# Kernel optimization log

Hardware: AMD Instinct MI355X
Metric: run time of the kernel (lower is better)

The kernel has to match this reference:

```python
import jax, jax.numpy as jnp
import numpy as np

N, E, NC, ES, NT, G = 200000, 500000, 150000, 350000, 100000, 1024
FN, FE, H, T = 133, 14, 128, 3


def _enc_params(key, prefix):
    ks = jax.random.split(key, 4)
    g = lambda k, shape, fan_in: jax.random.normal(k, shape, jnp.float32) / np.sqrt(fan_in).astype(np.float32)
    return {
        f"{prefix}_w_node": g(ks[0], (FN, H), FN),
        f"{prefix}_b_node": jnp.zeros((H,), jnp.float32),
        f"{prefix}_w_edge": g(ks[1], (FE, H), FE),
        f"{prefix}_b_edge": jnp.zeros((H,), jnp.float32),
        f"{prefix}_w_mp": g(ks[2], (T, H, H), H),
        f"{prefix}_b_mp": jnp.zeros((T, H), jnp.float32),
        f"{prefix}_w_out": g(ks[3], (H, H), H),
        f"{prefix}_b_out": jnp.zeros((H,), jnp.float32),
    }


def setup_inputs() -> dict:
    key = jax.random.key(0)
    k = lambda i: jax.random.fold_in(key, i)
    inp = {
        "x": jax.random.normal(k(0), (N, FN), jnp.float32),
        "node_weight": jax.random.uniform(k(1), (N,), jnp.float32),
        "edge_index": jax.random.randint(k(2), (2, E), 0, N),
        "edge_attr": jax.random.normal(k(3), (E, FE), jnp.float32),
        "edge_weight": jax.random.uniform(k(4), (E,), jnp.float32),
        "batch": jnp.sort(jax.random.randint(k(5), (N,), 0, G)),
        "context_nodes_mapper": jax.random.randint(k(6), (NC,), 0, N),
        "target_nodes_mapper": jax.random.randint(k(7), (NT,), 0, N),
        "combined_subgraphs": jax.random.randint(k(8), (2, ES), 0, NC),
        "subgraphs_edges_mapper": jax.random.randint(k(9), (ES,), 0, E),
        "context_edges_mask": jax.random.bernoulli(k(10), 0.7, (ES,)),
    }
    inp.update(_enc_params(k(11), "ctx"))
    inp.update(_enc_params(k(12), "tgt"))
    return inp


def wd_mpnn(x, src, dst, edge_attr, edge_weight, node_weight,
            w_node, b_node, w_edge, b_edge, w_mp, b_mp, w_out, b_out, n_nodes):
    # Weighted-edge node MPNN: gather source node states, combine with edge
    # embedding, scale by edge weight, scatter-sum onto destination nodes.
    h = jax.nn.relu(x @ w_node + b_node)                 # [n_nodes, H]
    eh = jax.nn.relu(edge_attr @ w_edge + b_edge)        # [n_edges, H]
    ew = edge_weight[:, None]
    for t in range(w_mp.shape[0]):
        msg = ew * (h[src] + eh)                         # gather [n_edges, H]
        agg = jax.ops.segment_sum(msg, dst, num_segments=n_nodes)
        h = jax.nn.relu(h + agg @ w_mp[t] + b_mp[t])
    return (h @ w_out + b_out) * node_weight[:, None]


def segment_mean(vals, seg, num_segments):
    s = jax.ops.segment_sum(vals, seg, num_segments=num_segments)
    c = jax.ops.segment_sum(jnp.ones((vals.shape[0],), vals.dtype), seg, num_segments=num_segments)
    return s / jnp.maximum(c, 1.0)[:, None]


def reference(x, node_weight, edge_index, edge_attr, edge_weight, batch,
              context_nodes_mapper, target_nodes_mapper, combined_subgraphs,
              subgraphs_edges_mapper, context_edges_mask,
              ctx_w_node, ctx_b_node, ctx_w_edge, ctx_b_edge, ctx_w_mp, ctx_b_mp, ctx_w_out, ctx_b_out,
              tgt_w_node, tgt_b_node, tgt_w_edge, tgt_b_edge, tgt_w_mp, tgt_b_mp, tgt_w_out, tgt_b_out):
    # --- context branch: gather subgraph node/edge features ---
    cx = x[context_nodes_mapper]                         # [NC, FN]
    cnw = node_weight[context_nodes_mapper]              # [NC]
    cea = edge_attr[subgraphs_edges_mapper]              # [ES, FE]
    # boolean edge mask folded into edge weights (messages scale linearly in
    # edge_weight, so zeroing masked edges == dropping them) -> jit friendly
    cew = edge_weight[subgraphs_edges_mapper] * context_edges_mask.astype(jnp.float32)
    csrc, cdst = combined_subgraphs[0], combined_subgraphs[1]
    ctx_nodes = wd_mpnn(cx, csrc, cdst, cea, cew, cnw,
                        ctx_w_node, ctx_b_node, ctx_w_edge, ctx_b_edge,
                        ctx_w_mp, ctx_b_mp, ctx_w_out, ctx_b_out, NC)
    ctx_emb = segment_mean(ctx_nodes, batch[context_nodes_mapper], G)   # [G, H]

    # --- target branch: full-graph encode, pool over target nodes ---
    full = wd_mpnn(x, edge_index[0], edge_index[1], edge_attr, edge_weight, node_weight,
                   tgt_w_node, tgt_b_node, tgt_w_edge, tgt_b_edge,
                   tgt_w_mp, tgt_b_mp, tgt_w_out, tgt_b_out, N)
    tgt_emb = segment_mean(full[target_nodes_mapper], batch[target_nodes_mapper], G)  # [G, H]

    return jnp.stack([ctx_emb, tgt_emb])                 # [2, G, H]
```

## Files before the change

kernel.cpp:

```cpp
#include <hip/hip_runtime.h>
#include <hip/hip_fp16.h>
#include <stdint.h>

#define H 128
#define FN 133
#define FE 14
#define NG 1024
#define APAD 133

typedef float v2f __attribute__((ext_vector_type(2)));

__device__ __forceinline__ uint2 pack_half4(float4 v) {
    __half2 a = __float22half2_rn(make_float2(v.x, v.y));
    __half2 b = __float22half2_rn(make_float2(v.z, v.w));
    uint2 r;
    r.x = *reinterpret_cast<unsigned int*>(&a);
    r.y = *reinterpret_cast<unsigned int*>(&b);
    return r;
}
__device__ __forceinline__ float4 unpack_half4(uint2 u) {
    __half2 a = *reinterpret_cast<__half2*>(&u.x);
    __half2 b = *reinterpret_cast<__half2*>(&u.y);
    float2 fa = __half22float2(a);
    float2 fb = __half22float2(b);
    return make_float4(fa.x, fa.y, fb.x, fb.y);
}

__global__ void k_sniff(const unsigned int* __restrict__ w, int nwords, int* __restrict__ flag) {
    __shared__ int sawFloat, sawBig;
    if (threadIdx.x == 0) { sawFloat = 0; sawBig = 0; }
    __syncthreads();
    int f = 0, bg = 0;
    for (int i = threadIdx.x; i < nwords; i += blockDim.x) {
        unsigned int v = w[i];
        if (v == 0u || v == 1u) continue;
        if (v == 0x3F800000u) f = 1; else bg = 1;
    }
    if (f) atomicOr(&sawFloat, 1);
    if (bg) atomicOr(&sawBig, 1);
    __syncthreads();
    if (threadIdx.x == 0) *flag = sawBig ? 1 : (sawFloat ? 2 : 0);
}

__device__ __forceinline__ float mask_val(const void* mask, int mm, long e) {
    if (mm == 1)      return ((const unsigned char*)mask)[e] ? 1.f : 0.f;
    else if (mm == 2) return ((const float*)mask)[e];
    else              return ((const int*)mask)[e] ? 1.f : 0.f;
}

template<bool GATHER>
__global__ __launch_bounds__(256)
void k_gemm_enc(const float* __restrict__ x, const int* __restrict__ map, int nrows,
                const float* __restrict__ w, const float* __restrict__ bias,
                float* __restrict__ hout) {
    __shared__ float w_lds[32][H];
    __shared__ float a_lds[32][APAD];
    __shared__ int   m_lds[128];
    const int tid = threadIdx.x;
    const int rbase = blockIdx.x * 128;
    if (GATHER && tid < 128) {
        int row = rbase + tid;
        m_lds[tid] = (row < nrows) ? map[row] : 0;
    }
    const int tx = tid & 15, ty = tid >> 4;
    float acc[8][8] = {};
    for (int kc = 0; kc < 5; ++kc) {
        const int k0 = kc * 32;
        __syncthreads();
        for (int i = tid; i < 32 * 32; i += 256) {
            int kk = i >> 5, c4 = i & 31;
            float4 v = make_float4(0.f, 0.f, 0.f, 0.f);
            if (k0 + kk < FN)
                v = reinterpret_cast<const float4*>(w + (size_t)(k0 + kk) * H)[c4];
            *reinterpret_cast<float4*>(&w_lds[kk][c4 * 4]) = v;
        }
        for (int i = tid; i < 128 * 32; i += 256) {
            int r = i >> 5, kk = i & 31;
            int row = rbase + r;
            float v = 0.f;
            if (row < nrows && k0 + kk < FN) {
                int sr = GATHER ? m_lds[r] : row;
                v = x[(size_t)sr * FN + k0 + kk];
            }
            a_lds[kk][r] = v;
        }
        __syncthreads();
        #pragma unroll 4
        for (int k = 0; k < 32; ++k) {
            float4 a0 = *reinterpret_cast<const float4*>(&a_lds[k][ty * 8]);
            float4 a1 = *reinterpret_cast<const float4*>(&a_lds[k][ty * 8 + 4]);
            float4 w0 = *reinterpret_cast<const float4*>(&w_lds[k][tx * 4]);
            float4 w1 = *reinterpret_cast<const float4*>(&w_lds[k][64 + tx * 4]);
            float aa[8] = {a0.x, a0.y, a0.z, a0.w, a1.x, a1.y, a1.z, a1.w};
            float ww[8] = {w0.x, w0.y, w0.z, w0.w, w1.x, w1.y, w1.z, w1.w};
            #pragma unroll
            for (int i2 = 0; i2 < 8; ++i2)
                #pragma unroll
                for (int j = 0; j < 8; ++j)
                    acc[i2][j] += aa[i2] * ww[j];
        }
    }
    float4 b0 = *reinterpret_cast<const float4*>(bias + tx * 4);
    float4 b1 = *reinterpret_cast<const float4*>(bias + 64 + tx * 4);
    float bb[8] = {b0.x, b0.y, b0.z, b0.w, b1.x, b1.y, b1.z, b1.w};
    #pragma unroll
    for (int i2 = 0; i2 < 8; ++i2) {
        int row = rbase + ty * 8 + i2;
        if (row < nrows) {
            float4 o0, o1;
            o0.x = fmaxf(acc[i2][0] + bb[0], 0.f); o0.y = fmaxf(acc[i2][1] + bb[1], 0.f);
            o0.z = fmaxf(acc[i2][2] + bb[2], 0.f); o0.w = fmaxf(acc[i2][3] + bb[3], 0.f);
            o1.x = fmaxf(acc[i2][4] + bb[4], 0.f); o1.y = fmaxf(acc[i2][5] + bb[5], 0.f);
            o1.z = fmaxf(acc[i2][6] + bb[6], 0.f); o1.w = fmaxf(acc[i2][7] + bb[7], 0.f);
            float* hp = hout + (size_t)row * H + tx * 4;
            *reinterpret_cast<float4*>(hp)      = o0;
            *reinterpret_cast<float4*>(hp + 64) = o1;
        }
    }
}

template<int MODE>
__global__ __launch_bounds__(256)
void k_hist(const int* __restrict__ dst, const float* __restrict__ edge_weight,
            const int* __restrict__ emap, const void* __restrict__ mask,
            const int* __restrict__ mmode_p, int* __restrict__ deg, int nedges) {
    int e = blockIdx.x * 256 + threadIdx.x;
    if (e >= nedges) return;
    int eo = MODE ? emap[e] : e;
    float w = edge_weight[eo];
    if (MODE) w *= mask_val(mask, *mmode_p, e);
    if (w != 0.f) atomicAdd(&deg[dst[e]], 1);
}

__global__ __launch_bounds__(256)
void k_scan1(const int* __restrict__ deg, int* __restrict__ off, int* __restrict__ bsum, int n) {
    __shared__ int tsum[256];
    const int tid = threadIdx.x;
    const int base = blockIdx.x * 1024;
    int local[4]; int s = 0;
    #pragma unroll
    for (int j = 0; j < 4; ++j) {
        int i = base + tid * 4 + j;
        local[j] = (i < n) ? deg[i] : 0;
        s += local[j];
    }
    tsum[tid] = s;
    __syncthreads();
    for (int d = 1; d < 256; d <<= 1) {
        int v = (tid >= d) ? tsum[tid - d] : 0;
        __syncthreads();
        tsum[tid] += v;
        __syncthreads();
    }
    int excl = tsum[tid] - s;
    #pragma unroll
    for (int j = 0; j < 4; ++j) {
        int i = base + tid * 4 + j;
        if (i < n) off[i] = excl;
        excl += local[j];
    }
    if (tid == 255) bsum[blockIdx.x] = tsum[255];
}

__global__ __launch_bounds__(256)
void k_scan2(int* __restrict__ bsum, int nb) {
    __shared__ int tsum[256];
    const int tid = threadIdx.x;
    int local[4]; int s = 0;
    #pragma unroll
    for (int j = 0; j < 4; ++j) {
        int i = tid * 4 + j;
        local[j] = (i < nb) ? bsum[i] : 0;
        s += local[j];
    }
    tsum[tid] = s;
    __syncthreads();
    for (int d = 1; d < 256; d <<= 1) {
        int v = (tid >= d) ? tsum[tid - d] : 0;
        __syncthreads();
        tsum[tid] += v;
        __syncthreads();
    }
    int excl = tsum[tid] - s;
    #pragma unroll
    for (int j = 0; j < 4; ++j) {
        int i = tid * 4 + j;
        if (i < nb) bsum[i] = excl;
        excl += local[j];
    }
}

__global__ __launch_bounds__(256)
void k_scan3(const int* __restrict__ bsum, int* __restrict__ off, int* __restrict__ cur, int n) {
    int i = blockIdx.x * 256 + threadIdx.x;
    if (i < n) {
        int o = off[i] + bsum[i >> 10];
        off[i] = o;
        cur[i] = o;
    }
}

template<int MODE>
__global__ __launch_bounds__(256)
void k_scatter(const int* __restrict__ src, const int* __restrict__ dst,
               const float* __restrict__ edge_weight,
               const int* __restrict__ emap, const void* __restrict__ mask,
               const int* __restrict__ mmode_p, int* __restrict__ cur,
               int2* __restrict__ epk, int2* __restrict__ epkh,
               int nedges) {
    int e = blockIdx.x * 256 + threadIdx.x;
    if (e >= nedges) return;
    int eo = MODE ? emap[e] : e;
    float w = edge_weight[eo];
    if (MODE) w *= mask_val(mask, *mmode_p, e);
    if (w != 0.f) {
        int pos = atomicAdd(&cur[dst[e]], 1);
        int wb = __float_as_int(w);
        epk[pos]  = make_int2(src[e], wb);
        epkh[pos] = make_int2(eo, wb);
    }
}

__global__ __launch_bounds__(256)
void k_mark(const int* __restrict__ rowmap, int* __restrict__ nflag, int nrows) {
    int r = blockIdx.x * 256 + threadIdx.x;
    if (r < nrows) nflag[rowmap[r]] = 1;
}

__global__ __launch_bounds__(256)
void k_compact(const int* __restrict__ nflag, int* __restrict__ list,
               int* __restrict__ cnt, int n) {
    int i = blockIdx.x * 256 + threadIdx.x;
    bool p = (i < n) && (nflag[i] != 0);
    unsigned long long m = __ballot(p);
    int lane = threadIdx.x & 63;
    int wcount = __popcll(m);
    int base = 0;
    if (lane == 0 && wcount) base = atomicAdd(cnt, wcount);
    base = __shfl(base, 0, 64);
    if (p) {
        int pos = base + (int)__popcll(m & ((1ull << lane) - 1ull));
        list[pos] = i;
    }
}

__global__ __launch_bounds__(256)
void k_msg_eh(const int* __restrict__ off, const int* __restrict__ deg,
              const int2* __restrict__ epk, const int2* __restrict__ epkh,
              const float* __restrict__ edge_attr,
              const float* __restrict__ w_edge, const float* __restrict__ b_edge,
              const float* __restrict__ h,
              __half* __restrict__ agg, __half* __restrict__ aggeh, int nnodes) {
    __shared__ float we_lds[FE * H];
    __shared__ float be_lds[H];
    for (int i = threadIdx.x; i < FE * H; i += 256) we_lds[i] = w_edge[i];
    if (threadIdx.x < H) be_lds[threadIdx.x] = b_edge[threadIdx.x];
    __syncthreads();
    const int hw = threadIdx.x >> 5;
    const int ln = threadIdx.x & 31;
    const int c  = ln * 4;
    int v = blockIdx.x * 8 + hw;
    if (v >= nnodes) return;
    v2f acc0 = {0.f, 0.f}, acc1 = {0.f, 0.f};
    v2f aeh0 = {0.f, 0.f}, aeh1 = {0.f, 0.f};
    const int o = off[v], d = deg[v];
    const float4 bev = *reinterpret_cast<const float4*>(be_lds + c);
    const v2f bev0 = {bev.x, bev.y}, bev1 = {bev.z, bev.w};
    for (int jb = 0; jb < d; jb += 32) {
        const int nn = min(32, d - jb);
        int2 m1 = make_int2(0, 0), m2 = make_int2(0, 0);
        if (ln < nn) { m1 = epk[o + jb + ln]; m2 = epkh[o + jb + ln]; }
        const int msrc = m1.x;
        const int meo  = m2.x;
        const float mw = __int_as_float(m1.y);
        for (int q = 0; q < nn; q += 2) {
            int   s0 = __shfl(msrc, q, 32);
            int   e0 = __shfl(meo,  q, 32);
            float w0 = __shfl(mw,   q, 32);
            int   s1 = __shfl(msrc, q + 1, 32);
            int   e1 = __shfl(meo,  q + 1, 32);
            float w1 = __shfl(mw,   q + 1, 32);
            if (q + 1 >= nn) { s1 = s0; e1 = e0; w1 = 0.f; }
            float4 hv0 = *reinterpret_cast<const float4*>(h + (size_t)s0 * H + c);
            float4 hv1 = *reinterpret_cast<const float4*>(h + (size_t)s1 * H + c);
            float a0 = (ln < FE) ? edge_attr[(size_t)e0 * FE + ln] : 0.f;
            float a1 = (ln < FE) ? edge_attr[(size_t)e1 * FE + ln] : 0.f;
            v2f eh00 = bev0, eh01 = bev1, eh10 = bev0, eh11 = bev1;
            #pragma unroll
            for (int k = 0; k < FE; ++k) {
                float f0 = __shfl(a0, k, 32);
                float f1 = __shfl(a1, k, 32);
                float4 wv = *reinterpret_cast<const float4*>(we_lds + k * H + c);
                v2f wva = {wv.x, wv.y}, wvb = {wv.z, wv.w};
                v2f f0v = {f0, f0}, f1v = {f1, f1};
                eh00 += f0v * wva; eh01 += f0v * wvb;
                eh10 += f1v * wva; eh11 += f1v * wvb;
            }
            v2f r00 = {w0 * fmaxf(eh00.x, 0.f), w0 * fmaxf(eh00.y, 0.f)};
            v2f r01 = {w0 * fmaxf(eh01.x, 0.f), w0 * fmaxf(eh01.y, 0.f)};
            v2f r10 = {w1 * fmaxf(eh10.x, 0.f), w1 * fmaxf(eh10.y, 0.f)};
            v2f r11 = {w1 * fmaxf(eh11.x, 0.f), w1 * fmaxf(eh11.y, 0.f)};
            aeh0 += r00 + r10; aeh1 += r01 + r11;
            v2f w0v = {w0, w0}, w1v = {w1, w1};
            acc0 += w0v * (v2f){hv0.x, hv0.y} + w1v * (v2f){hv1.x, hv1.y} + r00 + r10;
            acc1 += w0v * (v2f){hv0.z, hv0.w} + w1v * (v2f){hv1.z, hv1.w} + r01 + r11;
        }
    }
    *reinterpret_cast<uint2*>(agg   + (size_t)v * H + c) = pack_half4(make_float4(acc0.x, acc0.y, acc1.x, acc1.y));
    *reinterpret_cast<uint2*>(aggeh + (size_t)v * H + c) = pack_half4(make_float4(aeh0.x, aeh0.y, aeh1.x, aeh1.y));
}

template<int LIST>
__global__ __launch_bounds__(256)
void k_msg_csr(const int* __restrict__ off, const int* __restrict__ deg,
               const int2* __restrict__ epk, const __half* __restrict__ aggeh,
               const float* __restrict__ h, __half* __restrict__ agg,
               const int* __restrict__ list, const int* __restrict__ cnt_p,
               int nnodes) {
    const int hw = threadIdx.x >> 5;
    const int ln = threadIdx.x & 31;
    const int c  = ln * 4;
    int i = blockIdx.x * 8 + hw;
    int bound = LIST ? *cnt_p : nnodes;
    if (i >= bound) return;
    int v = LIST ? list[i] : i;
    float4 a0 = unpack_half4(*reinterpret_cast<const uint2*>(aggeh + (size_t)v * H + c));
    v2f acc0 = {a0.x, a0.y}, acc1 = {a0.z, a0.w};
    const int o = off[v], d = deg[v];
    for (int jb = 0; jb < d; jb += 32) {
        const int nn = min(32, d - jb);
        int2 meta = make_int2(0, 0);
        if (ln < nn) meta = epk[o + jb + ln];
        const int ms = meta.x;
        const float mw = __int_as_float(meta.y);
        for (int q = 0; q < nn; q += 4) {
            #pragma unroll
            for (int u = 0; u < 4; ++u) {
                int qq = q + u;
                int   s = __shfl(ms, qq, 32);
                float w = __shfl(mw, qq, 32);
                if (qq >= nn) { s = 0; w = 0.f; }
                float4 hv = *reinterpret_cast<const float4*>(h + (size_t)s * H + c);
                v2f wv = {w, w};
                acc0 += wv * (v2f){hv.x, hv.y};
                acc1 += wv * (v2f){hv.z, hv.w};
            }
        }
    }
    *reinterpret_cast<uint2*>(agg + (size_t)v * H + c) = pack_half4(make_float4(acc0.x, acc0.y, acc1.x, acc1.y));
}

template<int LIST>
__global__ __launch_bounds__(256)
void k_gemm_update(const __half* __restrict__ agg, int nrows,
                   const float* __restrict__ w, const float* __restrict__ bias,
                   float* __restrict__ h,
                   const int* __restrict__ list, const int* __restrict__ cnt_p) {
    __shared__ float w_lds[32][H];
    __shared__ float a_lds[32][APAD];
    __shared__ int   m_lds[128];
    const int tid = threadIdx.x;
    const int rbase = blockIdx.x * 128;
    const int bound = LIST ? *cnt_p : nrows;
    if (rbase >= bound) return;
    if (LIST && tid < 128) {
        int r = rbase + tid;
        m_lds[tid] = (r < bound) ? list[r] : 0;
    }
    const int tx = tid & 15, ty = tid >> 4;
    float acc[8][8] = {};
    for (int kc = 0; kc < 4; ++kc) {
        const int k0 = kc * 32;
        __syncthreads();
        for (int i = tid; i < 1024; i += 256) {
            int kk = i >> 5, c4 = i & 31;
            *reinterpret_cast<float4*>(&w_lds[kk][c4 * 4]) =
                reinterpret_cast<const float4*>(w + (size_t)(k0 + kk) * H)[c4];
        }
        for (int i = tid; i < 1024; i += 256) {
            int r = i >> 3, f = i & 7;
            int row = rbase + r;
            float4 v = make_float4(0.f, 0.f, 0.f, 0.f);
            if (row < bound) {
                int hr = LIST ? m_lds[r] : row;
                v = unpack_half4(reinterpret_cast<const uint2*>(agg + (size_t)hr * H + k0)[f]);
            }
            a_lds[f * 4 + 0][r] = v.x;
            a_lds[f * 4 + 1][r] = v.y;
            a_lds[f * 4 + 2][r] = v.z;
            a_lds[f * 4 + 3][r] = v.w;
        }
        __syncthreads();
        #pragma unroll 4
        for (int k = 0; k < 32; ++k) {
            float4 a0 = *reinterpret_cast<const float4*>(&a_lds[k][ty * 8]);
            float4 a1 = *reinterpret_cast<const float4*>(&a_lds[k][ty * 8 + 4]);
            float4 w0 = *reinterpret_cast<const float4*>(&w_lds[k][tx * 4]);
            float4 w1 = *reinterpret_cast<const float4*>(&w_lds[k][64 + tx * 4]);
            float aa[8] = {a0.x, a0.y, a0.z, a0.w, a1.x, a1.y, a1.z, a1.w};
            float ww[8] = {w0.x, w0.y, w0.z, w0.w, w1.x, w1.y, w1.z, w1.w};
            #pragma unroll
            for (int i2 = 0; i2 < 8; ++i2)
                #pragma unroll
                for (int j = 0; j < 8; ++j)
                    acc[i2][j] += aa[i2] * ww[j];
        }
    }
    float4 b0 = *reinterpret_cast<const float4*>(bias + tx * 4);
    float4 b1 = *reinterpret_cast<const float4*>(bias + 64 + tx * 4);
    float bb[8] = {b0.x, b0.y, b0.z, b0.w, b1.x, b1.y, b1.z, b1.w};
    #pragma unroll
    for (int i2 = 0; i2 < 8; ++i2) {
        int row = rbase + ty * 8 + i2;
        if (row < bound) {
            int hr = LIST ? m_lds[ty * 8 + i2] : row;
            float* hp = h + (size_t)hr * H + tx * 4;
            float4 h0 = *reinterpret_cast<const float4*>(hp);
            float4 h1 = *reinterpret_cast<const float4*>(hp + 64);
            float4 o0, o1;
            o0.x = fmaxf(h0.x + acc[i2][0] + bb[0], 0.f); o0.y = fmaxf(h0.y + acc[i2][1] + bb[1], 0.f);
            o0.z = fmaxf(h0.z + acc[i2][2] + bb[2], 0.f); o0.w = fmaxf(h0.w + acc[i2][3] + bb[3], 0.f);
            o1.x = fmaxf(h1.x + acc[i2][4] + bb[4], 0.f); o1.y = fmaxf(h1.y + acc[i2][5] + bb[5], 0.f);
            o1.z = fmaxf(h1.z + acc[i2][6] + bb[6], 0.f); o1.w = fmaxf(h1.w + acc[i2][7] + bb[7], 0.f);
            *reinterpret_cast<float4*>(hp)      = o0;
            *reinterpret_cast<float4*>(hp + 64) = o1;
        }
    }
}

__global__ __launch_bounds__(256)
void k_ghist(const int* __restrict__ rowmap, const int* __restrict__ batch,
             int* __restrict__ deg_g, int nrows) {
    int r = blockIdx.x * 256 + threadIdx.x;
    if (r < nrows) atomicAdd(&deg_g[batch[rowmap[r]]], 1);
}

__global__ __launch_bounds__(256)
void k_gscan(const int* __restrict__ deg, int* __restrict__ off, int* __restrict__ cur) {
    __shared__ int tsum[256];
    const int tid = threadIdx.x;
    int local[4]; int s = 0;
    #pragma unroll
    for (int j = 0; j < 4; ++j) { local[j] = deg[tid * 4 + j]; s += local[j]; }
    tsum[tid] = s;
    __syncthreads();
    for (int d = 1; d < 256; d <<= 1) {
        int v = (tid >= d) ? tsum[tid - d] : 0;
        __syncthreads();
        tsum[tid] += v;
        __syncthreads();
    }
    int excl = tsum[tid] - s;
    #pragma unroll
    for (int j = 0; j < 4; ++j) {
        off[tid * 4 + j] = excl;
        cur[tid * 4 + j] = excl;
        excl += local[j];
    }
}

template<bool GATHER>
__global__ __launch_bounds__(256)
void k_gscatter(const int* __restrict__ rowmap, const int* __restrict__ batch,
                const float* __restrict__ nodew, int* __restrict__ cur,
                int* __restrict__ prow, float* __restrict__ pnw, int nrows) {
    int r = blockIdx.x * 256 + threadIdx.x;
    if (r >= nrows) return;
    int oid = rowmap[r];
    int g = batch[oid];
    int pos = atomicAdd(&cur[g], 1);
    prow[pos] = GATHER ? oid : r;
    pnw[pos]  = nodew[oid];
}

__global__ __launch_bounds__(256)
void k_pool(const int* __restrict__ off_g, const int* __restrict__ deg_g,
            const int* __restrict__ prow, const float* __restrict__ pnw,
            const float* __restrict__ h,
            const float* __restrict__ w, const float* __restrict__ bias,
            float* __restrict__ outp) {
    __shared__ float s_lds[4][H];
    __shared__ float ssum[H];
    __shared__ float r_lds[2][H];
    __shared__ float cg_lds[4];
    const int g = blockIdx.x;
    const int o = off_g[g], cnt = deg_g[g];
    const int wv = threadIdx.x >> 6, lane = threadIdx.x & 63;
    float ax = 0.f, ay = 0.f, cg = 0.f;
    for (int i = wv; i < cnt; i += 4) {
        int hrow = prow[o + i];
        float nw = pnw[o + i];
        float2 v = *reinterpret_cast<const float2*>(h + (size_t)hrow * H + lane * 2);
        ax += nw * v.x; ay += nw * v.y; cg += nw;
    }
    s_lds[wv][lane * 2]     = ax;
    s_lds[wv][lane * 2 + 1] = ay;
    if (lane == 0) cg_lds[wv] = cg;
    __syncthreads();
    if (threadIdx.x < H)
        ssum[threadIdx.x] = s_lds[0][threadIdx.x] + s_lds[1][threadIdx.x]
                          + s_lds[2][threadIdx.x] + s_lds[3][threadIdx.x];
    __syncthreads();
    const int c = threadIdx.x & 127, kh = threadIdx.x >> 7;
    float p = 0.f;
    #pragma unroll 8
    for (int k = 0; k < 64; ++k)
        p += ssum[kh * 64 + k] * w[(size_t)(kh * 64 + k) * H + c];
    r_lds[kh][c] = p;
    __syncthreads();
    if (threadIdx.x < H) {
        float cga = cg_lds[0] + cg_lds[1] + cg_lds[2] + cg_lds[3];
        float val = r_lds[0][c] + r_lds[1][c] + bias[c] * cga;
        outp[(size_t)g * H + c] = val / fmaxf((float)cnt, 1.f);
    }
}

extern "C" void kernel_launch(void* const* d_in, const int* in_sizes, int n_in,
                              void* d_out, int out_size, void* d_ws, size_t ws_size,
                              hipStream_t stream) {
    (void)n_in; (void)out_size; (void)ws_size;
    const float* x           = (const float*)d_in[0];
    const float* node_weight = (const float*)d_in[1];
    const int*   edge_index  = (const int*)d_in[2];
    const float* edge_attr   = (const float*)d_in[3];
    const float* edge_weight = (const float*)d_in[4];
    const int*   batch       = (const int*)d_in[5];
    const int*   cnm         = (const int*)d_in[6];
    const int*   tnm         = (const int*)d_in[7];
    const int*   csub        = (const int*)d_in[8];
    const int*   sem         = (const int*)d_in[9];
    const void*  cmask       = d_in[10];

    const float* ctx_w_node = (const float*)d_in[11];
    const float* ctx_b_node = (const float*)d_in[12];
    const float* ctx_w_edge = (const float*)d_in[13];
    const float* ctx_b_edge = (const float*)d_in[14];
    const float* ctx_w_mp   = (const float*)d_in[15];
    const float* ctx_b_mp   = (const float*)d_in[16];
    const float* ctx_w_out  = (const float*)d_in[17];
    const float* ctx_b_out  = (const float*)d_in[18];
    const float* tgt_w_node = (const float*)d_in[19];
    const float* tgt_b_node = (const float*)d_in[20];
    const float* tgt_w_edge = (const float*)d_in[21];
    const float* tgt_b_edge = (const float*)d_in[22];
    const float* tgt_w_mp   = (const float*)d_in[23];
    const float* tgt_b_mp   = (const float*)d_in[24];
    const float* tgt_w_out  = (const float*)d_in[25];
    const float* tgt_b_out  = (const float*)d_in[26];

    const int N  = in_sizes[1];
    const int E  = in_sizes[4];
    const int NC = in_sizes[6];
    const int NT = in_sizes[7];
    const int ES = in_sizes[9];
    const int NMAX = (NT > NC) ? NT : NC;

    float* out = (float*)d_out;

    char* ws = (char*)d_ws;
    float*  h     = (float*)ws;  ws += (size_t)N * H * sizeof(float);
    __half* agg   = (__half*)ws; ws += (size_t)N * H * sizeof(__half);
    __half* aggeh = (__half*)ws; ws += (size_t)N * H * sizeof(__half);
    int2*  epk    = (int2*)ws;   ws += (size_t)E * sizeof(int2);
    int2*  epkh   = (int2*)ws;   ws += (size_t)E * sizeof(int2);
    int*   deg    = (int*)ws;    ws += (size_t)N * sizeof(int);
    int*   off    = (int*)ws;    ws += (size_t)N * sizeof(int);
    int*   cur    = (int*)ws;    ws += (size_t)N * sizeof(int);
    int*   nflag  = (int*)ws;    ws += (size_t)N * sizeof(int);
    int*   ncnt   = (int*)ws;    ws += sizeof(int);
    int*   nlist  = (int*)ws;    ws += (size_t)N * sizeof(int);
    int*   bsum   = (int*)ws;    ws += 1024 * sizeof(int);
    int*   deg_g  = (int*)ws;    ws += NG * sizeof(int);
    int*   off_g  = (int*)ws;    ws += NG * sizeof(int);
    int*   cur_g  = (int*)ws;    ws += NG * sizeof(int);
    int*   prow   = (int*)ws;    ws += (size_t)NMAX * sizeof(int);
    float* pnw    = (float*)ws;  ws += (size_t)NMAX * sizeof(float);
    int*   flag   = (int*)ws;    ws += sizeof(int);

    int nwords = ES / 4; if (nwords > 8192) nwords = 8192;
    k_sniff<<<1, 256, 0, stream>>>((const unsigned int*)cmask, nwords, flag);

    {
        const int* fsrc = edge_index;
        const int* fdst = edge_index + E;
        hipMemsetAsync(deg, 0, (size_t)N * sizeof(int), stream);
        hipMemsetAsync(nflag, 0, ((size_t)N + 1) * sizeof(int), stream);
        int egrid = (E + 255) / 256;
        k_hist<0><<<egrid, 256, 0, stream>>>(fdst, edge_weight, nullptr, nullptr, nullptr, deg, E);
        int nb1 = (N + 1023) / 1024;
        k_scan1<<<nb1, 256, 0, stream>>>(deg, off, bsum, N);
        k_scan2<<<1, 256, 0, stream>>>(bsum, nb1);
        k_scan3<<<(N + 255) / 256, 256, 0, stream>>>(bsum, off, cur, N);
        k_scatter<0><<<egrid, 256, 0, stream>>>(fsrc, fdst, edge_weight, nullptr, nullptr, nullptr,
                                                cur, epk, epkh, E);
        k_mark<<<(NT + 255) / 256, 256, 0, stream>>>(tnm, nflag, NT);
        k_compact<<<(N + 255) / 256, 256, 0, stream>>>(nflag, nlist, ncnt, N);

        k_gemm_enc<false><<<(N + 127) / 128, 256, 0, stream>>>(x, nullptr, N, tgt_w_node, tgt_b_node, h);
        k_msg_eh<<<(N + 7) / 8, 256, 0, stream>>>(off, deg, epk, epkh, edge_attr,
                                                  tgt_w_edge, tgt_b_edge, h, agg, aggeh, N);
        k_gemm_update<0><<<(N + 127) / 128, 256, 0, stream>>>(agg, N, tgt_w_mp, tgt_b_mp, h,
                                                              nullptr, nullptr);
        k_msg_csr<0><<<(N + 7) / 8, 256, 0, stream>>>(off, deg, epk, aggeh, h, agg, nullptr, nullptr, N);
        k_gemm_update<0><<<(N + 127) / 128, 256, 0, stream>>>(agg, N, tgt_w_mp + H * H, tgt_b_mp + H, h,
                                                              nullptr, nullptr);
        k_msg_csr<1><<<(N + 7) / 8, 256, 0, stream>>>(off, deg, epk, aggeh, h, agg, nlist, ncnt, N);
        k_gemm_update<1><<<(N + 127) / 128, 256, 0, stream>>>(agg, N, tgt_w_mp + 2 * H * H, tgt_b_mp + 2 * H, h,
                                                              nlist, ncnt);
        hipMemsetAsync(deg_g, 0, NG * sizeof(int), stream);
        k_ghist<<<(NT + 255) / 256, 256, 0, stream>>>(tnm, batch, deg_g, NT);
        k_gscan<<<1, 256, 0, stream>>>(deg_g, off_g, cur_g);
        k_gscatter<true><<<(NT + 255) / 256, 256, 0, stream>>>(tnm, batch, node_weight, cur_g, prow, pnw, NT);
        k_pool<<<NG, 256, 0, stream>>>(off_g, deg_g, prow, pnw, h, tgt_w_out, tgt_b_out,
                                       out + (size_t)NG * H);
    }

    {
        const int* csrc = csub;
        const int* cdst = csub + ES;
        hipMemsetAsync(deg, 0, (size_t)NC * sizeof(int), stream);
        int egrid = (ES + 255) / 256;
        k_hist<1><<<egrid, 256, 0, stream>>>(cdst, edge_weight, sem, cmask, flag, deg, ES);
        int nb1 = (NC + 1023) / 1024;
        k_scan1<<<nb1, 256, 0, stream>>>(deg, off, bsum, NC);
        k_scan2<<<1, 256, 0, stream>>>(bsum, nb1);
        k_scan3<<<(NC + 255) / 256, 256, 0, stream>>>(bsum, off, cur, NC);
        k_scatter<1><<<egrid, 256, 0, stream>>>(csrc, cdst, edge_weight, sem, cmask, flag,
                                                cur, epk, epkh, ES);
        k_gemm_enc<true><<<(NC + 127) / 128, 256, 0, stream>>>(x, cnm, NC, ctx_w_node, ctx_b_node, h);
        k_msg_eh<<<(NC + 7) / 8, 256, 0, stream>>>(off, deg, epk, epkh, edge_attr,
                                                   ctx_w_edge, ctx_b_edge, h, agg, aggeh, NC);
        k_gemm_update<0><<<(NC + 127) / 128, 256, 0, stream>>>(agg, NC, ctx_w_mp, ctx_b_mp, h,
                                                               nullptr, nullptr);
        for (int t = 1; t < 3; ++t) {
            k_msg_csr<0><<<(NC + 7) / 8, 256, 0, stream>>>(off, deg, epk, aggeh, h, agg, nullptr, nullptr, NC);
            k_gemm_update<0><<<(NC + 127) / 128, 256, 0, stream>>>(agg, NC,
                                                                   ctx_w_mp + t * H * H, ctx_b_mp + t * H, h,
                                                                   nullptr, nullptr);
        }
        hipMemsetAsync(deg_g, 0, NG * sizeof(int), stream);
        k_ghist<<<(NC + 255) / 256, 256, 0, stream>>>(cnm, batch, deg_g, NC);
        k_gscan<<<1, 256, 0, stream>>>(deg_g, off_g, cur_g);
        k_gscatter<false><<<(NC + 255) / 256, 256, 0, stream>>>(cnm, batch, node_weight, cur_g, prow, pnw, NC);
        k_pool<<<NG, 256, 0, stream>>>(off_g, deg_g, prow, pnw, h, ctx_w_out, ctx_b_out, out);
    }
}
```

Before: 1.499 ms.

## Restrict target branch's second MP round to two-hop neighborhood; shrink encoder GEMM tile

Adds a kernel that marks the target nodes plus all their in-edge source nodes, compacts that set, and runs the second message-passing round of the target branch only on those nodes. The final round already ran only on target nodes. Separately, the node-encoder GEMM tile drops from 128 to 64 rows per block, which doubles the grid and cuts registers and LDS per block. The reachability marking adds a serial per-node loop over edges, and the smaller tile reuses weights less.

```diff
diff --git a/kernel.cpp b/kernel.cpp
--- a/kernel.cpp
+++ b/kernel.cpp
@@ -54,27 +54,27 @@
                 const float* __restrict__ w, const float* __restrict__ bias,
                 float* __restrict__ hout) {
     __shared__ float w_lds[32][H];
-    __shared__ float a_lds[32][APAD];
-    __shared__ int   m_lds[128];
+    __shared__ float a_lds[32][69];
+    __shared__ int   m_lds[64];
     const int tid = threadIdx.x;
-    const int rbase = blockIdx.x * 128;
-    if (GATHER && tid < 128) {
+    const int rbase = blockIdx.x * 64;
+    if (GATHER && tid < 64) {
         int row = rbase + tid;
         m_lds[tid] = (row < nrows) ? map[row] : 0;
     }
     const int tx = tid & 15, ty = tid >> 4;
-    float acc[8][8] = {};
+    float acc[4][8] = {};
     for (int kc = 0; kc < 5; ++kc) {
         const int k0 = kc * 32;
         __syncthreads();
-        for (int i = tid; i < 32 * 32; i += 256) {
+        for (int i = tid; i < 1024; i += 256) {
             int kk = i >> 5, c4 = i & 31;
             float4 v = make_float4(0.f, 0.f, 0.f, 0.f);
             if (k0 + kk < FN)
                 v = reinterpret_cast<const float4*>(w + (size_t)(k0 + kk) * H)[c4];
             *reinterpret_cast<float4*>(&w_lds[kk][c4 * 4]) = v;
         }
-        for (int i = tid; i < 128 * 32; i += 256) {
+        for (int i = tid; i < 64 * 32; i += 256) {
             int r = i >> 5, kk = i & 31;
             int row = rbase + r;
             float v = 0.f;
@@ -87,14 +87,13 @@
         __syncthreads();
         #pragma unroll 4
         for (int k = 0; k < 32; ++k) {
-            float4 a0 = *reinterpret_cast<const float4*>(&a_lds[k][ty * 8]);
-            float4 a1 = *reinterpret_cast<const float4*>(&a_lds[k][ty * 8 + 4]);
+            float4 a0 = *reinterpret_cast<const float4*>(&a_lds[k][ty * 4]);
             float4 w0 = *reinterpret_cast<const float4*>(&w_lds[k][tx * 4]);
             float4 w1 = *reinterpret_cast<const float4*>(&w_lds[k][64 + tx * 4]);
-            float aa[8] = {a0.x, a0.y, a0.z, a0.w, a1.x, a1.y, a1.z, a1.w};
+            float aa[4] = {a0.x, a0.y, a0.z, a0.w};
             float ww[8] = {w0.x, w0.y, w0.z, w0.w, w1.x, w1.y, w1.z, w1.w};
             #pragma unroll
-            for (int i2 = 0; i2 < 8; ++i2)
+            for (int i2 = 0; i2 < 4; ++i2)
                 #pragma unroll
                 for (int j = 0; j < 8; ++j)
                     acc[i2][j] += aa[i2] * ww[j];
@@ -104,8 +103,8 @@
     float4 b1 = *reinterpret_cast<const float4*>(bias + 64 + tx * 4);
     float bb[8] = {b0.x, b0.y, b0.z, b0.w, b1.x, b1.y, b1.z, b1.w};
     #pragma unroll
-    for (int i2 = 0; i2 < 8; ++i2) {
-        int row = rbase + ty * 8 + i2;
+    for (int i2 = 0; i2 < 4; ++i2) {
+        int row = rbase + ty * 4 + i2;
         if (row < nrows) {
             float4 o0, o1;
             o0.x = fmaxf(acc[i2][0] + bb[0], 0.f); o0.y = fmaxf(acc[i2][1] + bb[1], 0.f);
@@ -242,6 +241,19 @@
         int pos = base + (int)__popcll(m & ((1ull << lane) - 1ull));
         list[pos] = i;
     }
+}
+
+__global__ __launch_bounds__(256)
+void k_mark_src(const int* __restrict__ off, const int* __restrict__ deg,
+                const int2* __restrict__ epk,
+                const int* __restrict__ list, const int* __restrict__ cnt_p,
+                int* __restrict__ nflag2) {
+    int i = blockIdx.x * 256 + threadIdx.x;
+    if (i >= *cnt_p) return;
+    int v = list[i];
+    nflag2[v] = 1;
+    const int o = off[v], d = deg[v];
+    for (int j = o; j < o + d; ++j) nflag2[epk[j].x] = 1;
 }
 
 __global__ __launch_bounds__(256)
@@ -568,7 +580,10 @@
     int*   cur    = (int*)ws;    ws += (size_t)N * sizeof(int);
     int*   nflag  = (int*)ws;    ws += (size_t)N * sizeof(int);
     int*   ncnt   = (int*)ws;    ws += sizeof(int);
+    int*   nflag2 = (int*)ws;    ws += (size_t)N * sizeof(int);
+    int*   ncnt2  = (int*)ws;    ws += sizeof(int);
     int*   nlist  = (int*)ws;    ws += (size_t)N * sizeof(int);
+    int*   nlist2 = (int*)ws;    ws += (size_t)N * sizeof(int);
     int*   bsum   = (int*)ws;    ws += 1024 * sizeof(int);
     int*   deg_g  = (int*)ws;    ws += NG * sizeof(int);
     int*   off_g  = (int*)ws;    ws += NG * sizeof(int);
@@ -584,7 +599,7 @@
         const int* fsrc = edge_index;
         const int* fdst = edge_index + E;
         hipMemsetAsync(deg, 0, (size_t)N * sizeof(int), stream);
-        hipMemsetAsync(nflag, 0, ((size_t)N + 1) * sizeof(int), stream);
+        hipMemsetAsync(nflag, 0, (2 * (size_t)N + 2) * sizeof(int), stream);
         int egrid = (E + 255) / 256;
         k_hist<0><<<egrid, 256, 0, stream>>>(fdst, edge_weight, nullptr, nullptr, nullptr, deg, E);
         int nb1 = (N + 1023) / 1024;
@@ -595,15 +610,17 @@
                                                 cur, epk, epkh, E);
         k_mark<<<(NT + 255) / 256, 256, 0, stream>>>(tnm, nflag, NT);
         k_compact<<<(N + 255) / 256, 256, 0, stream>>>(nflag, nlist, ncnt, N);
-
-        k_gemm_enc<false><<<(N + 127) / 128, 256, 0, stream>>>(x, nullptr, N, tgt_w_node, tgt_b_node, h);
+        k_mark_src<<<(N + 255) / 256, 256, 0, stream>>>(off, deg, epk, nlist, ncnt, nflag2);
+        k_compact<<<(N + 255) / 256, 256, 0, stream>>>(nflag2, nlist2, ncnt2, N);
+
+        k_gemm_enc<false><<<(N + 63) / 64, 256, 0, stream>>>(x, nullptr, N, tgt_w_node, tgt_b_node, h);
         k_msg_eh<<<(N + 7) / 8, 256, 0, stream>>>(off, deg, epk, epkh, edge_attr,
                                                   tgt_w_edge, tgt_b_edge, h, agg, aggeh, N);
         k_gemm_update<0><<<(N + 127) / 128, 256, 0, stream>>>(agg, N, tgt_w_mp, tgt_b_mp, h,
                                                               nullptr, nullptr);
-        k_msg_csr<0><<<(N + 7) / 8, 256, 0, stream>>>(off, deg, epk, aggeh, h, agg, nullptr, nullptr, N);
-        k_gemm_update<0><<<(N + 127) / 128, 256, 0, stream>>>(agg, N, tgt_w_mp + H * H, tgt_b_mp + H, h,
-                                                              nullptr, nullptr);
+        k_msg_csr<1><<<(N + 7) / 8, 256, 0, stream>>>(off, deg, epk, aggeh, h, agg, nlist2, ncnt2, N);
+        k_gemm_update<1><<<(N + 127) / 128, 256, 0, stream>>>(agg, N, tgt_w_mp + H * H, tgt_b_mp + H, h,
+                                                              nlist2, ncnt2);
         k_msg_csr<1><<<(N + 7) / 8, 256, 0, stream>>>(off, deg, epk, aggeh, h, agg, nlist, ncnt, N);
         k_gemm_update<1><<<(N + 127) / 128, 256, 0, stream>>>(agg, N, tgt_w_mp + 2 * H * H, tgt_b_mp + 2 * H, h,
                                                               nlist, ncnt);
@@ -627,7 +644,7 @@
         k_scan3<<<(NC + 255) / 256, 256, 0, stream>>>(bsum, off, cur, NC);
         k_scatter<1><<<egrid, 256, 0, stream>>>(csrc, cdst, edge_weight, sem, cmask, flag,
                                                 cur, epk, epkh, ES);
-        k_gemm_enc<true><<<(NC + 127) / 128, 256, 0, stream>>>(x, cnm, NC, ctx_w_node, ctx_b_node, h);
+        k_gemm_enc<true><<<(NC + 63) / 64, 256, 0, stream>>>(x, cnm, NC, ctx_w_node, ctx_b_node, h);
         k_msg_eh<<<(NC + 7) / 8, 256, 0, stream>>>(off, deg, epk, epkh, edge_attr,
                                                    ctx_w_edge, ctx_b_edge, h, agg, aggeh, NC);
         k_gemm_update<0><<<(NC + 127) / 128, 256, 0, stream>>>(agg, NC, ctx_w_mp, ctx_b_mp, h,
```

After: 1.496 ms. No clear change (-0.2%).
